# Kernel tuning notes

Measured on AMD Instinct MI355X. Metric: run time of the kernel, lower is better.

## Reference

```python
import jax, jax.numpy as jnp
import numpy as np

DIM = 2048
N_HEADS = 16
N_KV = 4
HEAD_DIM = DIM // N_HEADS  # 128
B, S = 2, 2048
EPS = float(np.finfo(np.float32).eps)  # torch RMSNorm eps=None -> finfo eps


def _rotate_half(x):
    # interleaved-pair rotation: out[..., ::2] = -x[..., 1::2]; out[..., 1::2] = x[..., ::2]
    x2 = x.reshape(x.shape[:-1] + (HEAD_DIM // 2, 2))
    rot = jnp.stack([-x2[..., 1], x2[..., 0]], axis=-1)
    return rot.reshape(x.shape)


def _rmsnorm(x, w):
    var = jnp.mean(x * x, axis=-1, keepdims=True)
    return x * jax.lax.rsqrt(var + EPS) * w


def setup_inputs() -> dict:
    key = jax.random.key(0)
    ks = jax.random.split(key, 5)
    out_f = (N_HEADS + 2 * N_KV) * HEAD_DIM  # 3072
    return {
        "x": jax.random.normal(ks[0], (B, S, DIM), jnp.float32),
        "wqkv": jax.random.normal(ks[1], (out_f, DIM), jnp.float32) * (2.0 / (DIM + out_f)) ** 0.5,
        "wo": jax.random.normal(ks[2], (DIM, DIM), jnp.float32) * (1.0 / DIM) ** 0.5,
        "q_norm_w": jnp.ones((HEAD_DIM,), jnp.float32),
        "k_norm_w": jnp.ones((HEAD_DIM,), jnp.float32),
        "freqs_cos": jnp.cos(jax.random.normal(ks[3], (S, 1, HEAD_DIM), jnp.float32)),
        "freqs_sin": jnp.sin(jax.random.normal(ks[4], (S, 1, HEAD_DIM), jnp.float32)),
    }


def reference(x, wqkv, wo, q_norm_w, k_norm_w, freqs_cos, freqs_sin):
    b, s, _ = x.shape
    qkv = jnp.einsum("bsd,od->bso", x, wqkv)
    q_size = N_HEADS * HEAD_DIM
    kv_size = N_KV * HEAD_DIM
    xq = qkv[..., :q_size].reshape(b, s, N_HEADS, HEAD_DIM)
    xk = qkv[..., q_size:q_size + kv_size].reshape(b, s, N_KV, HEAD_DIM)
    xv = qkv[..., q_size + kv_size:].reshape(b, s, N_KV, HEAD_DIM)
    xq = _rmsnorm(xq, q_norm_w)
    xk = _rmsnorm(xk, k_norm_w)
    # RoPE (freqs broadcast over batch and heads)
    xq = xq * freqs_cos + _rotate_half(xq) * freqs_sin
    xk = xk * freqs_cos + _rotate_half(xk) * freqs_sin
    # GQA: group query heads per kv head instead of materializing repeats
    rep = N_HEADS // N_KV
    q = xq.transpose(0, 2, 1, 3).reshape(b, N_KV, rep, s, HEAD_DIM)
    k = xk.transpose(0, 2, 1, 3)  # [b, kv, s, d]
    v = xv.transpose(0, 2, 1, 3)
    scale = 1.0 / jnp.sqrt(jnp.asarray(HEAD_DIM, x.dtype))
    scores = jnp.einsum("bhgqd,bhkd->bhgqk", q, k) * scale
    probs = jax.nn.softmax(scores, axis=-1)
    attn = jnp.einsum("bhgqk,bhkd->bhgqd", probs, v)
    attn = attn.reshape(b, N_HEADS, s, HEAD_DIM).transpose(0, 2, 1, 3).reshape(b, s, DIM)
    return jnp.einsum("bsd,od->bso", attn, wo)
```

## Files before the change

kernel.cpp:

```cpp
#include <hip/hip_runtime.h>
#include <hip/hip_bf16.h>

typedef unsigned short u16;
typedef __bf16 bf16x8 __attribute__((ext_vector_type(8)));
typedef __bf16 bf16x4 __attribute__((ext_vector_type(4)));
typedef u16 u16x8 __attribute__((ext_vector_type(8)));
typedef float f32x4 __attribute__((ext_vector_type(4)));
typedef float f32x16 __attribute__((ext_vector_type(16)));

__device__ __forceinline__ u16 f2bf(float f) {
    unsigned u = __float_as_uint(f);
    return (u16)((u + 0x7fffu + ((u >> 16) & 1u)) >> 16);
}
__device__ __forceinline__ unsigned pkbf2(float a, float b) {
    __hip_bfloat162 h = __float22bfloat162_rn(make_float2(a, b));
    return *(unsigned*)&h;
}

__device__ __forceinline__ void gload16(const u16* g, u16* l) {
    __builtin_amdgcn_global_load_lds(
        (const __attribute__((address_space(1))) void*)g,
        (__attribute__((address_space(3))) void*)l, 16, 0, 0);
}

__device__ __forceinline__ void block_sync() {
    __builtin_amdgcn_sched_barrier(0);
    __builtin_amdgcn_s_barrier();
    __builtin_amdgcn_sched_barrier(0);
}
template<int N> __device__ __forceinline__ void waitvm() {
    if constexpr (N == 0)      asm volatile("s_waitcnt vmcnt(0)" ::: "memory");
    else if constexpr (N == 6) asm volatile("s_waitcnt vmcnt(6)" ::: "memory");
    else                       asm volatile("s_waitcnt vmcnt(8)" ::: "memory");
}

__global__ void cvt_bf16(const float* __restrict__ src, u16* __restrict__ dst, int n4) {
    int i = blockIdx.x * 256 + threadIdx.x;
    if (i >= n4) return;
    float4 v = *(const float4*)(src + (size_t)i * 4);
    uint2 o; o.x = pkbf2(v.x, v.y); o.y = pkbf2(v.z, v.w);
    *(uint2*)(dst + (size_t)i * 4) = o;
}

template<int ROWS>
__device__ __forceinline__ void stage_tile(const u16* __restrict__ g, int K,
                                           int k0, u16* l, int tid) {
#pragma unroll
    for (int s = 0; s < ROWS / 64; ++s) {
        int row = s * 64 + (tid >> 3);
        int sc = (tid & 7) ^ ((tid >> 3) & 7);
        gload16(g + (size_t)row * K + k0 + sc * 8, l + s * 4096 + tid * 8);
    }
}

template<int BM, int BN>
__device__ __forceinline__ void gemm_pipeline(const u16* __restrict__ Ab,
                                              const u16* __restrict__ Bb, int K,
                                              u16* sAll,
                                              f32x4 (&acc)[BM / 32][BN / 64],
                                              int tid) {
    constexpr int MR = BM / 32, NR = BN / 64;
    constexpr int TILE = (BM + BN) * 64;
    const int lane = tid & 63, wave = tid >> 6;
    const int quad = lane >> 4, l16 = lane & 15;
    const int wm = wave >> 2, wn = wave & 3;
    const int ar0 = wm * (BM / 2) + l16;
    const int br0 = wn * (BN / 4) + l16;

    u16* sA0 = sAll;        u16* sB0 = sAll + BM * 64;
    u16* sA1 = sAll + TILE; u16* sB1 = sAll + TILE + BM * 64;

    stage_tile<BM>(Ab, K, 0, sA0, tid);
    stage_tile<BN>(Bb, K, 0, sB0, tid);

    const int nt = K >> 6;
    for (int t = 0; t < nt; ++t) {
        const u16* cA = (t & 1) ? sA1 : sA0;
        const u16* cB = (t & 1) ? sB1 : sB0;
        if (t + 1 < nt) {
            u16* nA = (t & 1) ? sA0 : sA1;
            u16* nB = (t & 1) ? sB0 : sB1;
            stage_tile<BM>(Ab, K, (t + 1) * 64, nA, tid);
            stage_tile<BN>(Bb, K, (t + 1) * 64, nB, tid);
            waitvm<(BM + BN) / 64>();
        } else {
            waitvm<0>();
        }
        block_sync();
#pragma unroll
        for (int kk = 0; kk < 2; ++kk) {
            const int c = kk * 4 + quad;
            bf16x8 af[MR], bf[NR];
#pragma unroll
            for (int m = 0; m < MR; ++m) {
                int r = ar0 + m * 16;
                af[m] = *(const bf16x8*)&cA[r * 64 + ((c ^ (r & 7)) * 8)];
            }
#pragma unroll
            for (int n = 0; n < NR; ++n) {
                int r = br0 + n * 16;
                bf[n] = *(const bf16x8*)&cB[r * 64 + ((c ^ (r & 7)) * 8)];
            }
            __builtin_amdgcn_s_setprio(1);
#pragma unroll
            for (int m = 0; m < MR; ++m)
#pragma unroll
                for (int n = 0; n < NR; ++n)
                    acc[m][n] = __builtin_amdgcn_mfma_f32_16x16x32_bf16(
                        af[m], bf[n], acc[m][n], 0, 0, 0);
            __builtin_amdgcn_s_setprio(0);
        }
        block_sync();
    }
}

__global__ __launch_bounds__(512, 2)
void gemm_bt(const u16* __restrict__ A, const u16* __restrict__ B,
             float* __restrict__ C, int M, int N, int K) {
    __shared__ u16 sAll[2 * (128 + 256) * 64];
    const int tid = threadIdx.x;
    const int wave = tid >> 6, lane = tid & 63;
    const int quad = lane >> 4, l16 = lane & 15;
    const int wm = wave >> 2, wn = wave & 3;
    const int bid = blockIdx.x;
    const int xcd = bid & 7, r2 = bid >> 3;
    const int bni = (xcd & 1) * 4 + (r2 & 3);
    const int bmi = (xcd >> 1) * 8 + (r2 >> 2);
    const size_t bm = (size_t)bmi * 128, bn = (size_t)bni * 256;
    f32x4 acc[4][4] = {};
    gemm_pipeline<128, 256>(A + bm * K, B + bn * K, K, sAll, acc, tid);
#pragma unroll
    for (int m = 0; m < 4; ++m)
#pragma unroll
        for (int n = 0; n < 4; ++n)
#pragma unroll
            for (int r = 0; r < 4; ++r)
                C[(bm + wm * 64 + m * 16 + quad * 4 + r) * (size_t)N +
                  bn + wn * 64 + n * 16 + l16] = acc[m][n][r];
}

__global__ __launch_bounds__(512, 2)
void gemm_qkv(const u16* __restrict__ xb, const u16* __restrict__ wq,
              const float* __restrict__ qw, const float* __restrict__ kw,
              const float* __restrict__ fcos, const float* __restrict__ fsin,
              u16* __restrict__ qb, u16* __restrict__ kb, u16* __restrict__ vt) {
    __shared__ u16 sAll[2 * (256 + 256) * 64];
    const int tid = threadIdx.x;
    const int wave = tid >> 6, lane = tid & 63;
    const int quad = lane >> 4, l16 = lane & 15;
    const int wm = wave >> 2, wn = wave & 3;
    const int bid = blockIdx.x;
    const int xcd = bid & 7, r2 = bid >> 3;
    const int bx = (xcd & 1) * 6 + r2 % 6;
    const int by = (xcd >> 1) * 4 + r2 / 6;
    f32x4 acc[8][4] = {};
    gemm_pipeline<256, 256>(xb + (size_t)by * 256 * 2048,
                            wq + (size_t)bx * 256 * 2048, 2048, sAll, acc, tid);

    const int b = by >> 3;
    const int sb = (by & 7) * 256 + wm * 128;
    const int headh = wn >> 1;
    const int dcol0 = (wn & 1) * 64;

    if (bx >= 10) {
        const int kvh = (bx - 10) * 2 + headh;
        u16* base = vt + (size_t)(b * 4 + kvh) * 128 * 2048;
#pragma unroll
        for (int m = 0; m < 8; ++m) {
            int s0 = sb + m * 16 + quad * 4;
#pragma unroll
            for (int n = 0; n < 4; ++n) {
                int d = dcol0 + n * 16 + l16;
                bf16x4 pv;
#pragma unroll
                for (int r = 0; r < 4; ++r) pv[r] = (__bf16)acc[m][n][r];
                *(bf16x4*)(base + (size_t)d * 2048 + s0) = pv;
            }
        }
        return;
    }

    float* red = (float*)sAll;
    float ssq[8][4];
#pragma unroll
    for (int m = 0; m < 8; ++m)
#pragma unroll
        for (int r = 0; r < 4; ++r) {
            float t = 0.f;
#pragma unroll
            for (int n = 0; n < 4; ++n) t += acc[m][n][r] * acc[m][n][r];
#pragma unroll
            for (int off = 1; off <= 8; off <<= 1) t += __shfl_xor(t, off);
            ssq[m][r] = t;
        }
    if (l16 == 0)
#pragma unroll
        for (int m = 0; m < 8; ++m)
#pragma unroll
            for (int r = 0; r < 4; ++r)
                red[((wn & 1) * 2 + headh) * 256 + wm * 128 + m * 16 + quad * 4 + r] =
                    ssq[m][r];
    __syncthreads();

    const bool isQ = bx < 8;
    const float qscl = isQ ? 0.08838834764831845f * 1.4426950408889634f : 1.0f;
    const float* wp = isQ ? qw : kw;
    float wcol[4];
#pragma unroll
    for (int n = 0; n < 4; ++n) wcol[n] = wp[dcol0 + n * 16 + l16];
    u16* dstbase = isQ ? qb + (size_t)(b * 16 + bx * 2 + headh) * 2048 * 128
                       : kb + (size_t)(b * 4 + (bx - 8) * 2 + headh) * 2048 * 128;
    const float sgn = (l16 & 1) ? 1.f : -1.f;

#pragma unroll
    for (int m = 0; m < 8; ++m) {
#pragma unroll
        for (int r = 0; r < 4; ++r) {
            int rowl = wm * 128 + m * 16 + quad * 4 + r;
            float var = (red[(0 + headh) * 256 + rowl] +
                         red[(2 + headh) * 256 + rowl]) * (1.0f / 128.0f);
            float rms = rsqrtf(var + 1.1920928955078125e-07f) * qscl;
            int s = sb + m * 16 + quad * 4 + r;
            const float* fc = fcos + (size_t)s * 128 + dcol0;
            const float* fn = fsin + (size_t)s * 128 + dcol0;
            u16* drow = dstbase + (size_t)s * 128 + dcol0;
#pragma unroll
            for (int n = 0; n < 4; ++n) {
                float y = acc[m][n][r] * rms * wcol[n];
                float yp = __shfl_xor(y, 1);
                float o = y * fc[n * 16 + l16] + sgn * yp * fn[n * 16 + l16];
                drow[n * 16 + l16] = f2bf(o);
            }
        }
    }
}

#define KBUF(c) ((c) * 8192)
#define VBUF(c) (16384 + (c) * 8192)
__global__ __launch_bounds__(256, 2)
void flash_attn(const u16* __restrict__ qb, const u16* __restrict__ kb,
                const u16* __restrict__ vt, u16* __restrict__ ab) {
    __shared__ u16 smem[32768];
    __shared__ float Llds[128];

    const int tid = threadIdx.x;
    const int wave = tid >> 6, lane = tid & 63;
    const int hf = lane >> 5, c32 = lane & 31;
    const int bid = blockIdx.x;
    const int swz = (bid & 7) * 64 + (bid >> 3);
    const int qt = swz & 15, bh = swz >> 4;
    const int hh = bh & 15, bb = bh >> 4;
    const int kh = hh >> 2;

    const u16* Qbase = qb + (size_t)(bb * 16 + hh) * 2048 * 128;
    const u16* Kbase = kb + (size_t)(bb * 4 + kh) * 2048 * 128;
    const u16* Vbase = vt + (size_t)(bb * 4 + kh) * 128 * 2048;

    bf16x8 aq[8];
#pragma unroll
    for (int kq = 0; kq < 8; ++kq)
        aq[kq] = *(const bf16x8*)(Qbase +
            (size_t)(qt * 128 + wave * 32 + c32) * 128 + kq * 16 + hf * 8);

    f32x16 O[4] = {};
    float lacc = 0.f;

    const int st_key = tid >> 4, st_c16 = tid & 15;
    const int st_d = tid >> 3, st_c8 = tid & 7;

    u16x8 kreg[4], vreg[4];
#pragma unroll
    for (int it = 0; it < 4; ++it) {
        int key = st_key + it * 16, d = st_d + it * 32;
        kreg[it] = *(const u16x8*)(Kbase + (size_t)key * 128 + st_c16 * 8);
        vreg[it] = *(const u16x8*)(Vbase + (size_t)d * 2048 + st_c8 * 8);
    }
#pragma unroll
    for (int it = 0; it < 4; ++it) {
        int key = st_key + it * 16, d = st_d + it * 32;
        *(u16x8*)&smem[KBUF(0) + key * 128 + ((st_c16 ^ (key & 7)) * 8)] = kreg[it];
        *(u16x8*)&smem[VBUF(0) + d * 64 + ((st_c8 ^ (d & 7)) * 8)] = vreg[it];
    }
    __syncthreads();

    for (int kt = 0; kt < 32; ++kt) {
        const int cur = kt & 1, nxt = cur ^ 1;
        if (kt < 31) {
            const int key0n = (kt + 1) * 64;
#pragma unroll
            for (int it = 0; it < 4; ++it) {
                int key = st_key + it * 16, d = st_d + it * 32;
                kreg[it] = *(const u16x8*)(Kbase + (size_t)(key0n + key) * 128 + st_c16 * 8);
                vreg[it] = *(const u16x8*)(Vbase + (size_t)d * 2048 + key0n + st_c8 * 8);
            }
        }

        f32x16 sc[2] = {};
        __builtin_amdgcn_s_setprio(1);
#pragma unroll
        for (int kq = 0; kq < 8; ++kq) {
#pragma unroll
            for (int mt = 0; mt < 2; ++mt) {
                bf16x8 kf = *(const bf16x8*)&smem[KBUF(cur) + (mt * 32 + c32) * 128 +
                                                 (((kq * 2 + hf) ^ (c32 & 7)) * 8)];
                sc[mt] = __builtin_amdgcn_mfma_f32_32x32x16_bf16(kf, aq[kq], sc[mt], 0, 0, 0);
            }
        }
        __builtin_amdgcn_s_setprio(0);

        int pdw[2][8];
#pragma unroll
        for (int mt = 0; mt < 2; ++mt) {
            float p[16];
#pragma unroll
            for (int r = 0; r < 16; ++r) {
                p[r] = __builtin_amdgcn_exp2f(sc[mt][r]);
                lacc += p[r];
            }
#pragma unroll
            for (int i = 0; i < 8; ++i) pdw[mt][i] = (int)pkbf2(p[2 * i], p[2 * i + 1]);
        }

        if (kt < 31) {
#pragma unroll
            for (int it = 0; it < 4; ++it) {
                int key = st_key + it * 16, d = st_d + it * 32;
                *(u16x8*)&smem[KBUF(nxt) + key * 128 + ((st_c16 ^ (key & 7)) * 8)] = kreg[it];
                *(u16x8*)&smem[VBUF(nxt) + d * 64 + ((st_c8 ^ (d & 7)) * 8)] = vreg[it];
            }
        }

#pragma unroll
        for (int kc = 0; kc < 4; ++kc) {
            const int mt = kc >> 1, L = kc & 1;
            int s0 = hf ? pdw[mt][4 * L + 0] : pdw[mt][4 * L + 2];
            int s1 = hf ? pdw[mt][4 * L + 1] : pdw[mt][4 * L + 3];
            int r0 = __shfl_xor(s0, 32);
            int r1 = __shfl_xor(s1, 32);
            union { int i[4]; bf16x8 v; } u;
            u.i[0] = hf ? r0 : pdw[mt][4 * L + 0];
            u.i[1] = hf ? r1 : pdw[mt][4 * L + 1];
            u.i[2] = hf ? pdw[mt][4 * L + 2] : r0;
            u.i[3] = hf ? pdw[mt][4 * L + 3] : r1;
            __builtin_amdgcn_s_setprio(1);
#pragma unroll
            for (int dt = 0; dt < 4; ++dt) {
                bf16x8 vf = *(const bf16x8*)&smem[VBUF(cur) + (dt * 32 + c32) * 64 +
                                                 (((kc * 2 + hf) ^ (c32 & 7)) * 8)];
                O[dt] = __builtin_amdgcn_mfma_f32_32x32x16_bf16(u.v, vf, O[dt], 0, 0, 0);
            }
            __builtin_amdgcn_s_setprio(0);
        }
        __syncthreads();
    }

    float l = lacc + __shfl_xor(lacc, 32);
    if (hf == 0) Llds[wave * 32 + c32] = l;

    float inv[16];
#pragma unroll
    for (int r = 0; r < 16; ++r)
        inv[r] = __builtin_amdgcn_rcpf(Llds[wave * 32 + (r & 3) + 8 * (r >> 2) + 4 * hf]);

    u16* scr = &smem[wave * 32 * 136];
#pragma unroll
    for (int dt = 0; dt < 4; ++dt)
#pragma unroll
        for (int r = 0; r < 16; ++r) {
            int q_r = (r & 3) + 8 * (r >> 2) + 4 * hf;
            scr[q_r * 136 + dt * 32 + c32] = f2bf(O[dt][r] * inv[r]);
        }
#pragma unroll
    for (int it = 0; it < 8; ++it) {
        int f = it * 64 + lane;
        int row = f >> 4, c = f & 15;
        u16x8 v = *(const u16x8*)&scr[row * 136 + c * 8];
        int qg = qt * 128 + wave * 32 + row;
        *(u16x8*)(ab + ((size_t)(bb * 2048 + qg)) * 2048 + hh * 128 + c * 8) = v;
    }
}

extern "C" void kernel_launch(void* const* d_in, const int* in_sizes, int n_in,
                              void* d_out, int out_size, void* d_ws, size_t ws_size,
                              hipStream_t stream) {
    const float* x    = (const float*)d_in[0];
    const float* wqkv = (const float*)d_in[1];
    const float* wo   = (const float*)d_in[2];
    const float* qw   = (const float*)d_in[3];
    const float* kw   = (const float*)d_in[4];
    const float* fc   = (const float*)d_in[5];
    const float* fs   = (const float*)d_in[6];
    float* out = (float*)d_out;
    char* ws = (char*)d_ws;

    u16* xb    = (u16*)(ws + 0);
    u16* wqkvb = (u16*)(ws + 16777216);
    u16* wob   = (u16*)(ws + 29360128);
    u16* qb    = (u16*)(ws + 37748736);
    u16* kb    = (u16*)(ws + 54525952);
    u16* vt    = (u16*)(ws + 58720256);
    u16* ab    = (u16*)(ws + 62914560);

    cvt_bf16<<<8192, 256, 0, stream>>>(x, xb, 2097152);
    cvt_bf16<<<6144, 256, 0, stream>>>(wqkv, wqkvb, 1572864);
    cvt_bf16<<<4096, 256, 0, stream>>>(wo, wob, 1048576);
    gemm_qkv<<<192, 512, 0, stream>>>(xb, wqkvb, qw, kw, fc, fs, qb, kb, vt);
    flash_attn<<<512, 256, 0, stream>>>(qb, kb, vt, ab);
    gemm_bt<<<256, 512, 0, stream>>>(ab, wob, out, 4096, 2048, 2048);
}
```

Before: 313.4 us.

## Stage K/V tiles via async global-to-LDS loads and permute V layout to drop shuffles

The attention loop now stages K and V tiles directly into LDS with global_load_lds, with the XOR swizzle folded into the global address, instead of round-tripping through registers. A wait on the vm counter plus a block sync replaces the register-held prefetch. The V-transpose write in the QKV kernel permutes sequence positions by quad so the P operand can be packed straight from registers, removing the per-chunk cross-lane shuffles. This frees registers and VALU/LDS-store work, but relies on the V layout permutation exactly matching the MFMA operand order.

```diff
diff --git a/kernel.cpp b/kernel.cpp
--- a/kernel.cpp
+++ b/kernel.cpp
@@ -163,11 +163,12 @@
     const int dcol0 = (wn & 1) * 64;
 
     if (bx >= 10) {
+        const int qp = ((quad & 1) << 1) | (quad >> 1);
         const int kvh = (bx - 10) * 2 + headh;
         u16* base = vt + (size_t)(b * 4 + kvh) * 128 * 2048;
 #pragma unroll
         for (int m = 0; m < 8; ++m) {
-            int s0 = sb + m * 16 + quad * 4;
+            int s0 = sb + m * 16 + qp * 4;
 #pragma unroll
             for (int n = 0; n < 4; ++n) {
                 int d = dcol0 + n * 16 + l16;
@@ -265,35 +266,30 @@
     f32x16 O[4] = {};
     float lacc = 0.f;
 
-    const int st_key = tid >> 4, st_c16 = tid & 15;
-    const int st_d = tid >> 3, st_c8 = tid & 7;
-
-    u16x8 kreg[4], vreg[4];
-#pragma unroll
-    for (int it = 0; it < 4; ++it) {
-        int key = st_key + it * 16, d = st_d + it * 32;
-        kreg[it] = *(const u16x8*)(Kbase + (size_t)key * 128 + st_c16 * 8);
-        vreg[it] = *(const u16x8*)(Vbase + (size_t)d * 2048 + st_c8 * 8);
-    }
-#pragma unroll
-    for (int it = 0; it < 4; ++it) {
-        int key = st_key + it * 16, d = st_d + it * 32;
-        *(u16x8*)&smem[KBUF(0) + key * 128 + ((st_c16 ^ (key & 7)) * 8)] = kreg[it];
-        *(u16x8*)&smem[VBUF(0) + d * 64 + ((st_c8 ^ (d & 7)) * 8)] = vreg[it];
-    }
-    __syncthreads();
+    const int krow = tid >> 4;
+    const u16* kg = Kbase + (size_t)krow * 128 + (((tid & 15) ^ (krow & 7)) * 8);
+    const int vrow = tid >> 3;
+    const u16* vg = Vbase + (size_t)vrow * 2048 + (((tid & 7) ^ (vrow & 7)) * 8);
+
+    auto stage = [&](int buf, int key0) {
+#pragma unroll
+        for (int s = 0; s < 4; ++s) {
+            gload16(kg + key0 * 128 + s * 2048, &smem[KBUF(buf) + s * 2048 + tid * 8]);
+            gload16(vg + (size_t)s * 65536 + key0, &smem[VBUF(buf) + s * 2048 + tid * 8]);
+        }
+    };
+
+    stage(0, 0);
 
     for (int kt = 0; kt < 32; ++kt) {
         const int cur = kt & 1, nxt = cur ^ 1;
         if (kt < 31) {
-            const int key0n = (kt + 1) * 64;
-#pragma unroll
-            for (int it = 0; it < 4; ++it) {
-                int key = st_key + it * 16, d = st_d + it * 32;
-                kreg[it] = *(const u16x8*)(Kbase + (size_t)(key0n + key) * 128 + st_c16 * 8);
-                vreg[it] = *(const u16x8*)(Vbase + (size_t)d * 2048 + key0n + st_c8 * 8);
-            }
-        }
+            stage(nxt, (kt + 1) * 64);
+            waitvm<8>();
+        } else {
+            waitvm<0>();
+        }
+        block_sync();
 
         f32x16 sc[2] = {};
         __builtin_amdgcn_s_setprio(1);
@@ -321,37 +317,24 @@
             for (int i = 0; i < 8; ++i) pdw[mt][i] = (int)pkbf2(p[2 * i], p[2 * i + 1]);
         }
 
-        if (kt < 31) {
-#pragma unroll
-            for (int it = 0; it < 4; ++it) {
-                int key = st_key + it * 16, d = st_d + it * 32;
-                *(u16x8*)&smem[KBUF(nxt) + key * 128 + ((st_c16 ^ (key & 7)) * 8)] = kreg[it];
-                *(u16x8*)&smem[VBUF(nxt) + d * 64 + ((st_c8 ^ (d & 7)) * 8)] = vreg[it];
-            }
-        }
-
+        __builtin_amdgcn_s_setprio(1);
 #pragma unroll
         for (int kc = 0; kc < 4; ++kc) {
             const int mt = kc >> 1, L = kc & 1;
-            int s0 = hf ? pdw[mt][4 * L + 0] : pdw[mt][4 * L + 2];
-            int s1 = hf ? pdw[mt][4 * L + 1] : pdw[mt][4 * L + 3];
-            int r0 = __shfl_xor(s0, 32);
-            int r1 = __shfl_xor(s1, 32);
             union { int i[4]; bf16x8 v; } u;
-            u.i[0] = hf ? r0 : pdw[mt][4 * L + 0];
-            u.i[1] = hf ? r1 : pdw[mt][4 * L + 1];
-            u.i[2] = hf ? pdw[mt][4 * L + 2] : r0;
-            u.i[3] = hf ? pdw[mt][4 * L + 3] : r1;
-            __builtin_amdgcn_s_setprio(1);
+            u.i[0] = pdw[mt][4 * L + 0];
+            u.i[1] = pdw[mt][4 * L + 1];
+            u.i[2] = pdw[mt][4 * L + 2];
+            u.i[3] = pdw[mt][4 * L + 3];
 #pragma unroll
             for (int dt = 0; dt < 4; ++dt) {
                 bf16x8 vf = *(const bf16x8*)&smem[VBUF(cur) + (dt * 32 + c32) * 64 +
                                                  (((kc * 2 + hf) ^ (c32 & 7)) * 8)];
                 O[dt] = __builtin_amdgcn_mfma_f32_32x32x16_bf16(u.v, vf, O[dt], 0, 0, 0);
             }
-            __builtin_amdgcn_s_setprio(0);
-        }
-        __syncthreads();
+        }
+        __builtin_amdgcn_s_setprio(0);
+        block_sync();
     }
 
     float l = lacc + __shfl_xor(lacc, 32);
```

Result: faster. 305.2 us (-2.6%).
